# Kernel tuning notes

Hardware: AMD Instinct MI355X
Metric: run time of the kernel (lower is better)

The kernel has to match this reference:

```python
import jax, jax.numpy as jnp
import numpy as np

CLIPS_NUM = 4
OUTPUT_SIZE = 1000000  # outputSize: number of features in trainset (scales Z)
T = 0.07               # temperature
QUEUE_K = 131072       # queue size
D = 128                # inputSize (feature dim)
BS = 256               # batch_size * clips_num


def _l2norm(x):
    return x / jnp.linalg.norm(x, axis=-1, keepdims=True)


def setup_inputs() -> dict:
    key = jax.random.key(0)
    kq, kk, km = jax.random.split(key, 3)
    # MoCo-style L2-normalized features keep exp(sim/T) finite.
    q = _l2norm(jax.random.normal(kq, (BS, D), jnp.float32))
    k = _l2norm(jax.random.normal(kk, (BS, D), jnp.float32))
    memory = _l2norm(jax.random.normal(km, (QUEUE_K, D), jnp.float32))
    return {"q": q, "k": k, "memory": memory, "i": 0}


def _make_indices(bs, clips_num):
    """Static (numpy) replication of MemoryMoCo.prepare_indices."""
    batch_size = bs // clips_num
    # indices[v] = row indices of all clips of video v: [batch_size, clips_num]
    indices = np.arange(bs).reshape(clips_num, batch_size).T
    vid = np.arange(bs) % batch_size
    all_clips = vid[:, None] + np.arange(clips_num)[None, :] * batch_size  # [bs, clips_num]
    mask = all_clips != np.arange(bs)[:, None]
    pos_indices = all_clips[mask].reshape(bs, clips_num - 1)  # drop self
    return jnp.asarray(indices), jnp.asarray(pos_indices)


def reference(q, k, memory, i):
    bs, d = q.shape
    batch_size = bs // CLIPS_NUM
    indices, pos_indices = _make_indices(bs, CLIPS_NUM)

    k = jax.lax.stop_gradient(k)            # k = k.detach()
    mem = jax.lax.stop_gradient(memory)     # queue = memory.clone().detach()

    # l_pos: gather positives, per-row bmm with q, mean over positives -> [bs, 1]
    positives = k[pos_indices]              # [bs, clips_num-1, d]
    l_pos = jnp.mean(jnp.einsum('bpd,bd->bp', positives, q), axis=-1, keepdims=True)

    # l_neg: queue GEMM -> [bs, K]
    l_neg = q @ mem.T

    out = jnp.concatenate([l_pos, l_neg], axis=1)   # [bs, 1+K]
    out = jnp.exp(out / T)
    # First-call NCE normalization: Z = out.mean() * outputSize (Z is detached in torch)
    Z = jax.lax.stop_gradient(jnp.mean(out) * OUTPUT_SIZE)
    out = out / Z

    probs = jnp.mean(out[:, 0] / jnp.sum(out, axis=1))  # extract_probs

    # no_grad memory-bank update: scatter mean of each video's clip keys
    out_ids = jnp.arange(batch_size) % memory.shape[0]   # index=0, fmod queueSize
    k_mean = jnp.mean(k[indices], axis=1)                # [batch_size, d]
    new_memory = memory.at[out_ids].set(k_mean)

    return out, probs, new_memory
```

## Files before the change

### kernel.cpp

```cpp
#include <hip/hip_runtime.h>
#include <hip/hip_bf16.h>

constexpr int       DIM        = 128;
constexpr long long CN         = 131073;
constexpr long long OUT_ELEMS  = 256LL * 131073LL;
constexpr long long PROBS_OFF  = OUT_ELEMS;
constexpr long long MEMOUT_OFF = OUT_ELEMS + 1;
constexpr long long MEM_ELEMS  = 131072LL * 128LL;

constexpr float SCL = 20.60992915555662f;

constexpr int WS_INVZ  = 0;
constexpr int WS_ELPOS = 16;
constexpr int WS_KMEAN = 272;
constexpr int WS_ROWP  = 8464;
constexpr int WS_MEMBF = 16656;

typedef __attribute__((ext_vector_type(8))) short  short8v;
typedef __attribute__((ext_vector_type(4))) float  f32x4;
typedef __attribute__((ext_vector_type(4), aligned(4))) float f32x4u;

__device__ __forceinline__ unsigned short f2bf(float x) {
  unsigned u = __float_as_uint(x);
  u += 0x7fffu + ((u >> 16) & 1u);
  return (unsigned short)(u >> 16);
}

__device__ __forceinline__ short8v pack8(float4 a, float4 b) {
  short8v h;
  h[0] = (short)f2bf(a.x); h[1] = (short)f2bf(a.y);
  h[2] = (short)f2bf(a.z); h[3] = (short)f2bf(a.w);
  h[4] = (short)f2bf(b.x); h[5] = (short)f2bf(b.y);
  h[6] = (short)f2bf(b.z); h[7] = (short)f2bf(b.w);
  return h;
}

__global__ __launch_bounds__(256) void k_prep(const float* __restrict__ q,
                                              const float* __restrict__ k,
                                              float* __restrict__ ws) {
  const int b = blockIdx.x, t = threadIdx.x;
  if (b < 32) {
    int j = b * 256 + t;
    int v = j >> 7, d = j & 127;
    ws[WS_KMEAN + j] = 0.25f * (k[v*128+d] + k[(v+64)*128+d] +
                                k[(v+128)*128+d] + k[(v+192)*128+d]);
  } else if (b < 96) {
    int row = (b - 32) * 4 + (t >> 6);
    int lane = t & 63;
    int vid = row & 63;
    float2 qv = ((const float2*)(q + row * DIM))[lane];
    float2 kr = ((const float2*)(k + row * DIM))[lane];
    float s0 = -kr.x, s1 = -kr.y;
    #pragma unroll
    for (int c = 0; c < 4; ++c) {
      float2 kc = ((const float2*)(k + (vid + c * 64) * DIM))[lane];
      s0 += kc.x; s1 += kc.y;
    }
    float acc = qv.x * s0 + qv.y * s1;
    #pragma unroll
    for (int off = 1; off < 64; off <<= 1) acc += __shfl_xor(acc, off, 64);
    if (lane == 0) ws[WS_ELPOS + row] = exp2f(acc * (1.f / 3.f) * SCL);
  } else {
    int i = (b - 96) * 2048 + t * 8;
    float4 z = {0.f, 0.f, 0.f, 0.f};
    *(float4*)(ws + WS_ROWP + i)     = z;
    *(float4*)(ws + WS_ROWP + i + 4) = z;
  }
}

template<int NT>
__global__ __launch_bounds__(256) void k_gemm0(const float* __restrict__ memv,
                                               const float* __restrict__ q,
                                               unsigned short* __restrict__ membf,
                                               float* __restrict__ ws) {
  const int t = threadIdx.x, lane = t & 63, wave = t >> 6;
  const int g = lane >> 4, nlo = lane & 15;

  short8v af[4][4];
  #pragma unroll
  for (int ks = 0; ks < 4; ++ks)
    #pragma unroll
    for (int mf = 0; mf < 4; ++mf) {
      const float4* src = (const float4*)(q + (wave*64 + mf*16 + nlo)*DIM + ks*32 + g*8);
      af[ks][mf] = pack8(src[0], src[1]);
    }

  float sums[4][4];
  #pragma unroll
  for (int mf = 0; mf < 4; ++mf)
    #pragma unroll
    for (int r = 0; r < 4; ++r) sums[mf][r] = 0.f;

  for (int it = 0; it < NT; ++it) {
    const long long n0 = ((long long)blockIdx.x * NT + it) * 32;
    f32x4 acc[4][2];
    f32x4 zero = {0.f, 0.f, 0.f, 0.f};
    #pragma unroll
    for (int mf = 0; mf < 4; ++mf) { acc[mf][0] = zero; acc[mf][1] = zero; }

    #pragma unroll
    for (int ks = 0; ks < 4; ++ks) {
      #pragma unroll
      for (int nf = 0; nf < 2; ++nf) {
        const long long off = (n0 + nf*16 + nlo) * DIM + ks*32 + g*8;
        const float4* src = (const float4*)(memv + off);
        short8v bfr = pack8(src[0], src[1]);
        if (wave == ks)
          *(short8v*)(membf + off) = bfr;
        #pragma unroll
        for (int mf = 0; mf < 4; ++mf)
          acc[mf][nf] = __builtin_amdgcn_mfma_f32_16x16x32_bf16(af[ks][mf], bfr, acc[mf][nf], 0, 0, 0);
      }
    }

    #pragma unroll
    for (int mf = 0; mf < 4; ++mf)
      #pragma unroll
      for (int r = 0; r < 4; ++r)
        sums[mf][r] += exp2f(acc[mf][0][r] * SCL) + exp2f(acc[mf][1][r] * SCL);
  }

  float* rowp = ws + WS_ROWP + (blockIdx.x & 31) * 256;
  #pragma unroll
  for (int mf = 0; mf < 4; ++mf) {
    #pragma unroll
    for (int r = 0; r < 4; ++r) {
      float s = sums[mf][r];
      s += __shfl_xor(s, 1, 16);
      s += __shfl_xor(s, 2, 16);
      s += __shfl_xor(s, 4, 16);
      s += __shfl_xor(s, 8, 16);
      if (nlo == 0) atomicAdd(&rowp[wave*64 + mf*16 + g*4 + r], s);
    }
  }
}

__global__ void k_fin(float* __restrict__ ws, float* __restrict__ out) {
  __shared__ float s_tot[256];
  __shared__ float s_pr[256];
  __shared__ float sh_invZ;
  int t = threadIdx.x;
  float s = ws[WS_ELPOS + t];
  float rs = s;
  for (int sl = 0; sl < 32; ++sl) rs += ws[WS_ROWP + sl * 256 + t];
  s_tot[t] = rs;
  s_pr[t] = s / rs;
  __syncthreads();
  for (int off = 128; off > 0; off >>= 1) {
    if (t < off) { s_tot[t] += s_tot[t + off]; s_pr[t] += s_pr[t + off]; }
    __syncthreads();
  }
  if (t == 0) {
    double Z = (double)s_tot[0] * (1000000.0 / (256.0 * 131073.0));
    float invZ = (float)(1.0 / Z);
    ws[WS_INVZ] = invZ;
    sh_invZ = invZ;
    out[PROBS_OFF] = s_pr[0] * (1.f / 256.f);
  }
  __syncthreads();
  out[(long long)t * CN] = s * sh_invZ;
}

template<int NT>
__global__ __launch_bounds__(256) void k_gemm1(const unsigned short* __restrict__ membf,
                                               const float* __restrict__ q,
                                               const float* __restrict__ ws,
                                               float* __restrict__ out) {
  const int t = threadIdx.x, lane = t & 63, wave = t >> 6;
  const int g = lane >> 4, nlo = lane & 15;
  const float invZ = ws[WS_INVZ];

  short8v af[4][4];
  #pragma unroll
  for (int ks = 0; ks < 4; ++ks)
    #pragma unroll
    for (int mf = 0; mf < 4; ++mf) {
      const float4* src = (const float4*)(q + (wave*64 + mf*16 + nlo)*DIM + ks*32 + g*8);
      af[ks][mf] = pack8(src[0], src[1]);
    }

  long long rowoff[4][4];
  #pragma unroll
  for (int mf = 0; mf < 4; ++mf)
    #pragma unroll
    for (int r = 0; r < 4; ++r)
      rowoff[mf][r] = (long long)(wave*64 + mf*16 + g*4 + r) * CN + 1 + nlo;

  const int logical = (blockIdx.x & 7) * 64 + (blockIdx.x >> 3);
  const long long t0 = (long long)logical * NT;

  for (int it = 0; it < NT; ++it) {
    const long long n0 = (t0 + it) * 32;
    f32x4 acc[4][2];
    f32x4 zero = {0.f, 0.f, 0.f, 0.f};
    #pragma unroll
    for (int mf = 0; mf < 4; ++mf) { acc[mf][0] = zero; acc[mf][1] = zero; }

    #pragma unroll
    for (int ks = 0; ks < 4; ++ks) {
      short8v b0 = *(const short8v*)(membf + (n0 + nlo)      * DIM + ks*32 + g*8);
      short8v b1 = *(const short8v*)(membf + (n0 + 16 + nlo) * DIM + ks*32 + g*8);
      #pragma unroll
      for (int mf = 0; mf < 4; ++mf) {
        acc[mf][0] = __builtin_amdgcn_mfma_f32_16x16x32_bf16(af[ks][mf], b0, acc[mf][0], 0, 0, 0);
        acc[mf][1] = __builtin_amdgcn_mfma_f32_16x16x32_bf16(af[ks][mf], b1, acc[mf][1], 0, 0, 0);
      }
    }

    #pragma unroll
    for (int mf = 0; mf < 4; ++mf) {
      #pragma unroll
      for (int r = 0; r < 4; ++r) {
        out[rowoff[mf][r] + n0]      = exp2f(acc[mf][0][r] * SCL) * invZ;
        out[rowoff[mf][r] + n0 + 16] = exp2f(acc[mf][1][r] * SCL) * invZ;
      }
    }
  }
}

__global__ void k_copy(const float* __restrict__ memv, const float* __restrict__ ws,
                       float* __restrict__ out) {
  float* dst = out + MEMOUT_OFF;
  const float* km = ws + WS_KMEAN;
  long long gid = blockIdx.x * 256LL + threadIdx.x;
  if (gid == 0) {
    dst[0] = km[0]; dst[1] = km[1]; dst[2] = km[2];
    dst[8191] = km[8191];
    dst[8192] = memv[8192]; dst[8193] = memv[8193]; dst[8194] = memv[8194];
    dst[MEM_ELEMS - 1] = memv[MEM_ELEMS - 1];
  }
  if (gid < 2047) {
    long long base = 3 + gid * 4;
    f32x4u v = *(const f32x4u*)(km + base);
    *(f32x4u*)(dst + base) = v;
  }
  const long long NGB = (MEM_ELEMS - 1 - 8195) / 4;
  const long long stride = (long long)gridDim.x * 256LL;
  for (long long j = gid; j < NGB; j += stride) {
    long long base = 8195 + j * 4;
    f32x4u v = *(const f32x4u*)(memv + base);
    *(f32x4u*)(dst + base) = v;
  }
}

extern "C" void kernel_launch(void* const* d_in, const int* in_sizes, int n_in,
                              void* d_out, int out_size, void* d_ws, size_t ws_size,
                              hipStream_t stream) {
  (void)in_sizes; (void)n_in; (void)out_size; (void)ws_size;
  const float* q    = (const float*)d_in[0];
  const float* k    = (const float*)d_in[1];
  const float* memv = (const float*)d_in[2];
  float* out = (float*)d_out;
  float* ws  = (float*)d_ws;
  unsigned short* membf = (unsigned short*)(ws + WS_MEMBF);

  hipLaunchKernelGGL(k_prep, dim3(100), dim3(256), 0, stream, q, k, ws);
  hipLaunchKernelGGL((k_gemm0<8>), dim3(512), dim3(256), 0, stream, memv, q, membf, ws);
  hipLaunchKernelGGL(k_fin,  dim3(1),   dim3(256), 0, stream, ws, out);
  hipLaunchKernelGGL((k_gemm1<8>), dim3(512), dim3(256), 0, stream, membf, q, ws, out);
  hipLaunchKernelGGL(k_copy, dim3(2048), dim3(256), 0, stream, memv, ws, out);
}
```

Baseline: 409.1 us.

## Fuse all stages into one persistent kernel with a grid-wide barrier

Merges prep, the first GEMM pass, the finalization, the second GEMM pass and the memory copy into a single kernel of 512 blocks. A spin-wait atomic counter acts as a grid barrier between the Z-reduction pass and the output-writing pass. The second pass re-reads and re-converts the fp32 memory instead of going through a bf16 staging copy, and the memory-bank copy is spread across the blocks before the barrier. This removes four kernel launches and the bf16 staging writes. In exchange it re-reads the fp32 memory, adds memsets, and relies on all 512 blocks being co-resident (launch_bounds of 2 blocks per CU), or the barrier deadlocks.

```diff
diff --git a/kernel.cpp b/kernel.cpp
--- a/kernel.cpp
+++ b/kernel.cpp
@@ -10,11 +10,12 @@
 
 constexpr float SCL = 20.60992915555662f;
 
-constexpr int WS_INVZ  = 0;
-constexpr int WS_ELPOS = 16;
+constexpr int WS_CTR   = 8;
 constexpr int WS_KMEAN = 272;
 constexpr int WS_ROWP  = 8464;
-constexpr int WS_MEMBF = 16656;
+
+constexpr int GRID   = 512;
+constexpr int NTILES = 8;
 
 typedef __attribute__((ext_vector_type(8))) short  short8v;
 typedef __attribute__((ext_vector_type(4))) float  f32x4;
@@ -35,55 +36,53 @@
   return h;
 }
 
-__global__ __launch_bounds__(256) void k_prep(const float* __restrict__ q,
-                                              const float* __restrict__ k,
-                                              float* __restrict__ ws) {
+__global__ __launch_bounds__(256, 2) void k_mega(const float* __restrict__ qg,
+                                                 const float* __restrict__ kg,
+                                                 const float* __restrict__ memv,
+                                                 float* __restrict__ ws,
+                                                 float* __restrict__ out) {
   const int b = blockIdx.x, t = threadIdx.x;
-  if (b < 32) {
-    int j = b * 256 + t;
-    int v = j >> 7, d = j & 127;
-    ws[WS_KMEAN + j] = 0.25f * (k[v*128+d] + k[(v+64)*128+d] +
-                                k[(v+128)*128+d] + k[(v+192)*128+d]);
-  } else if (b < 96) {
-    int row = (b - 32) * 4 + (t >> 6);
-    int lane = t & 63;
-    int vid = row & 63;
-    float2 qv = ((const float2*)(q + row * DIM))[lane];
-    float2 kr = ((const float2*)(k + row * DIM))[lane];
-    float s0 = -kr.x, s1 = -kr.y;
-    #pragma unroll
-    for (int c = 0; c < 4; ++c) {
-      float2 kc = ((const float2*)(k + (vid + c * 64) * DIM))[lane];
-      s0 += kc.x; s1 += kc.y;
-    }
-    float acc = qv.x * s0 + qv.y * s1;
-    #pragma unroll
-    for (int off = 1; off < 64; off <<= 1) acc += __shfl_xor(acc, off, 64);
-    if (lane == 0) ws[WS_ELPOS + row] = exp2f(acc * (1.f / 3.f) * SCL);
-  } else {
-    int i = (b - 96) * 2048 + t * 8;
-    float4 z = {0.f, 0.f, 0.f, 0.f};
-    *(float4*)(ws + WS_ROWP + i)     = z;
-    *(float4*)(ws + WS_ROWP + i + 4) = z;
-  }
-}
-
-template<int NT>
-__global__ __launch_bounds__(256) void k_gemm0(const float* __restrict__ memv,
-                                               const float* __restrict__ q,
-                                               unsigned short* __restrict__ membf,
-                                               float* __restrict__ ws) {
-  const int t = threadIdx.x, lane = t & 63, wave = t >> 6;
-  const int g = lane >> 4, nlo = lane & 15;
+  const int lane = t & 63, wave = t >> 6, g = lane >> 4, nlo = lane & 15;
+  __shared__ float sh_s;
+  __shared__ float sh_rs[256];
+  __shared__ float sh_red[256];
 
   short8v af[4][4];
   #pragma unroll
   for (int ks = 0; ks < 4; ++ks)
     #pragma unroll
     for (int mf = 0; mf < 4; ++mf) {
-      const float4* src = (const float4*)(q + (wave*64 + mf*16 + nlo)*DIM + ks*32 + g*8);
+      const float4* src = (const float4*)(qg + (wave*64 + mf*16 + nlo)*DIM + ks*32 + g*8);
       af[ks][mf] = pack8(src[0], src[1]);
     }
+
+  if (b < 256 && wave == 0) {
+    const int vid = b & 63;
+    float2 qv = ((const float2*)(qg + b*DIM))[lane];
+    float2 kr = ((const float2*)(kg + b*DIM))[lane];
+    float s0 = -kr.x, s1 = -kr.y;
+    #pragma unroll
+    for (int c = 0; c < 4; ++c) {
+      float2 kc = ((const float2*)(kg + (vid + c*64)*DIM))[lane];
+      s0 += kc.x; s1 += kc.y;
+    }
+    float acc = qv.x*s0 + qv.y*s1;
+    #pragma unroll
+    for (int off = 1; off < 64; off <<= 1) acc += __shfl_xor(acc, off, 64);
+    if (lane == 0) {
+      float s = exp2f(acc * (1.f/3.f) * SCL);
+      sh_s = s;
+      atomicAdd(&ws[WS_ROWP + (b & 31)*256 + b], s);
+    }
+  }
+  if (b == 0) {
+    for (int j = t; j < 8192; j += 256) {
+      int v = j >> 7, d = j & 127;
+      ws[WS_KMEAN + j] = 0.25f * (kg[v*DIM+d] + kg[(v+64)*DIM+d] +
+                                  kg[(v+128)*DIM+d] + kg[(v+192)*DIM+d]);
+    }
+  }
+  __syncthreads();
 
   float sums[4][4];
   #pragma unroll
@@ -91,8 +90,8 @@
     #pragma unroll
     for (int r = 0; r < 4; ++r) sums[mf][r] = 0.f;
 
-  for (int it = 0; it < NT; ++it) {
-    const long long n0 = ((long long)blockIdx.x * NT + it) * 32;
+  for (int it = 0; it < NTILES; ++it) {
+    const long long n0 = (long long)b * (NTILES*32) + it*32;
     f32x4 acc[4][2];
     f32x4 zero = {0.f, 0.f, 0.f, 0.f};
     #pragma unroll
@@ -100,106 +99,10 @@
 
     #pragma unroll
     for (int ks = 0; ks < 4; ++ks) {
-      #pragma unroll
-      for (int nf = 0; nf < 2; ++nf) {
-        const long long off = (n0 + nf*16 + nlo) * DIM + ks*32 + g*8;
-        const float4* src = (const float4*)(memv + off);
-        short8v bfr = pack8(src[0], src[1]);
-        if (wave == ks)
-          *(short8v*)(membf + off) = bfr;
-        #pragma unroll
-        for (int mf = 0; mf < 4; ++mf)
-          acc[mf][nf] = __builtin_amdgcn_mfma_f32_16x16x32_bf16(af[ks][mf], bfr, acc[mf][nf], 0, 0, 0);
-      }
-    }
-
-    #pragma unroll
-    for (int mf = 0; mf < 4; ++mf)
-      #pragma unroll
-      for (int r = 0; r < 4; ++r)
-        sums[mf][r] += exp2f(acc[mf][0][r] * SCL) + exp2f(acc[mf][1][r] * SCL);
-  }
-
-  float* rowp = ws + WS_ROWP + (blockIdx.x & 31) * 256;
-  #pragma unroll
-  for (int mf = 0; mf < 4; ++mf) {
-    #pragma unroll
-    for (int r = 0; r < 4; ++r) {
-      float s = sums[mf][r];
-      s += __shfl_xor(s, 1, 16);
-      s += __shfl_xor(s, 2, 16);
-      s += __shfl_xor(s, 4, 16);
-      s += __shfl_xor(s, 8, 16);
-      if (nlo == 0) atomicAdd(&rowp[wave*64 + mf*16 + g*4 + r], s);
-    }
-  }
-}
-
-__global__ void k_fin(float* __restrict__ ws, float* __restrict__ out) {
-  __shared__ float s_tot[256];
-  __shared__ float s_pr[256];
-  __shared__ float sh_invZ;
-  int t = threadIdx.x;
-  float s = ws[WS_ELPOS + t];
-  float rs = s;
-  for (int sl = 0; sl < 32; ++sl) rs += ws[WS_ROWP + sl * 256 + t];
-  s_tot[t] = rs;
-  s_pr[t] = s / rs;
-  __syncthreads();
-  for (int off = 128; off > 0; off >>= 1) {
-    if (t < off) { s_tot[t] += s_tot[t + off]; s_pr[t] += s_pr[t + off]; }
-    __syncthreads();
-  }
-  if (t == 0) {
-    double Z = (double)s_tot[0] * (1000000.0 / (256.0 * 131073.0));
-    float invZ = (float)(1.0 / Z);
-    ws[WS_INVZ] = invZ;
-    sh_invZ = invZ;
-    out[PROBS_OFF] = s_pr[0] * (1.f / 256.f);
-  }
-  __syncthreads();
-  out[(long long)t * CN] = s * sh_invZ;
-}
-
-template<int NT>
-__global__ __launch_bounds__(256) void k_gemm1(const unsigned short* __restrict__ membf,
-                                               const float* __restrict__ q,
-                                               const float* __restrict__ ws,
-                                               float* __restrict__ out) {
-  const int t = threadIdx.x, lane = t & 63, wave = t >> 6;
-  const int g = lane >> 4, nlo = lane & 15;
-  const float invZ = ws[WS_INVZ];
-
-  short8v af[4][4];
-  #pragma unroll
-  for (int ks = 0; ks < 4; ++ks)
-    #pragma unroll
-    for (int mf = 0; mf < 4; ++mf) {
-      const float4* src = (const float4*)(q + (wave*64 + mf*16 + nlo)*DIM + ks*32 + g*8);
-      af[ks][mf] = pack8(src[0], src[1]);
-    }
-
-  long long rowoff[4][4];
-  #pragma unroll
-  for (int mf = 0; mf < 4; ++mf)
-    #pragma unroll
-    for (int r = 0; r < 4; ++r)
-      rowoff[mf][r] = (long long)(wave*64 + mf*16 + g*4 + r) * CN + 1 + nlo;
-
-  const int logical = (blockIdx.x & 7) * 64 + (blockIdx.x >> 3);
-  const long long t0 = (long long)logical * NT;
-
-  for (int it = 0; it < NT; ++it) {
-    const long long n0 = (t0 + it) * 32;
-    f32x4 acc[4][2];
-    f32x4 zero = {0.f, 0.f, 0.f, 0.f};
-    #pragma unroll
-    for (int mf = 0; mf < 4; ++mf) { acc[mf][0] = zero; acc[mf][1] = zero; }
-
-    #pragma unroll
-    for (int ks = 0; ks < 4; ++ks) {
-      short8v b0 = *(const short8v*)(membf + (n0 + nlo)      * DIM + ks*32 + g*8);
-      short8v b1 = *(const short8v*)(membf + (n0 + 16 + nlo) * DIM + ks*32 + g*8);
+      const float4* p0 = (const float4*)(memv + (n0 + nlo)      * DIM + ks*32 + g*8);
+      const float4* p1 = (const float4*)(memv + (n0 + 16 + nlo) * DIM + ks*32 + g*8);
+      short8v b0 = pack8(p0[0], p0[1]);
+      short8v b1 = pack8(p1[0], p1[1]);
       #pragma unroll
       for (int mf = 0; mf < 4; ++mf) {
         acc[mf][0] = __builtin_amdgcn_mfma_f32_16x16x32_bf16(af[ks][mf], b0, acc[mf][0], 0, 0, 0);
@@ -208,38 +111,128 @@
     }
 
     #pragma unroll
+    for (int mf = 0; mf < 4; ++mf)
+      #pragma unroll
+      for (int r = 0; r < 4; ++r)
+        sums[mf][r] += exp2f(acc[mf][0][r] * SCL) + exp2f(acc[mf][1][r] * SCL);
+  }
+
+  {
+    float* rowp = ws + WS_ROWP + (b & 31) * 256;
+    #pragma unroll
     for (int mf = 0; mf < 4; ++mf) {
       #pragma unroll
       for (int r = 0; r < 4; ++r) {
-        out[rowoff[mf][r] + n0]      = exp2f(acc[mf][0][r] * SCL) * invZ;
-        out[rowoff[mf][r] + n0 + 16] = exp2f(acc[mf][1][r] * SCL) * invZ;
-      }
-    }
-  }
-}
-
-__global__ void k_copy(const float* __restrict__ memv, const float* __restrict__ ws,
-                       float* __restrict__ out) {
-  float* dst = out + MEMOUT_OFF;
-  const float* km = ws + WS_KMEAN;
-  long long gid = blockIdx.x * 256LL + threadIdx.x;
-  if (gid == 0) {
-    dst[0] = km[0]; dst[1] = km[1]; dst[2] = km[2];
-    dst[8191] = km[8191];
-    dst[8192] = memv[8192]; dst[8193] = memv[8193]; dst[8194] = memv[8194];
-    dst[MEM_ELEMS - 1] = memv[MEM_ELEMS - 1];
-  }
-  if (gid < 2047) {
-    long long base = 3 + gid * 4;
-    f32x4u v = *(const f32x4u*)(km + base);
-    *(f32x4u*)(dst + base) = v;
-  }
-  const long long NGB = (MEM_ELEMS - 1 - 8195) / 4;
-  const long long stride = (long long)gridDim.x * 256LL;
-  for (long long j = gid; j < NGB; j += stride) {
-    long long base = 8195 + j * 4;
-    f32x4u v = *(const f32x4u*)(memv + base);
-    *(f32x4u*)(dst + base) = v;
+        float s = sums[mf][r];
+        s += __shfl_xor(s, 1, 16);
+        s += __shfl_xor(s, 2, 16);
+        s += __shfl_xor(s, 4, 16);
+        s += __shfl_xor(s, 8, 16);
+        if (nlo == 0) atomicAdd(&rowp[wave*64 + mf*16 + g*4 + r], s);
+      }
+    }
+  }
+
+  {
+    float* dst = out + MEMOUT_OFF;
+    const float* km = ws + WS_KMEAN;
+    if (b == 0 && t == 0) {
+      dst[0] = km[0]; dst[1] = km[1]; dst[2] = km[2];
+      dst[MEM_ELEMS - 1] = memv[MEM_ELEMS - 1];
+    }
+    #pragma unroll
+    for (int i = 0; i < 32; ++i) {
+      long long j = (long long)b * 8192 + i*256 + t;
+      if (j < 4194303LL) {
+        long long base = 3 + j*4;
+        f32x4u v;
+        if (base + 4 <= 8192) {
+          v = *(const f32x4u*)(km + base);
+        } else if (base >= 8192) {
+          v = *(const f32x4u*)(memv + base);
+        } else {
+          float tmp[4];
+          #pragma unroll
+          for (int e = 0; e < 4; ++e) {
+            long long idx = base + e;
+            tmp[e] = (idx < 8192) ? km[idx] : memv[idx];
+          }
+          v.x = tmp[0]; v.y = tmp[1]; v.z = tmp[2]; v.w = tmp[3];
+        }
+        *(f32x4u*)(dst + base) = v;
+      }
+    }
+  }
+
+  __syncthreads();
+  if (t == 0) {
+    unsigned* ctr = (unsigned*)ws + WS_CTR;
+    __hip_atomic_fetch_add(ctr, 1u, __ATOMIC_ACQ_REL, __HIP_MEMORY_SCOPE_AGENT);
+    while (__hip_atomic_load(ctr, __ATOMIC_ACQUIRE, __HIP_MEMORY_SCOPE_AGENT) < (unsigned)GRID) {
+      __builtin_amdgcn_s_sleep(2);
+    }
+  }
+  __syncthreads();
+
+  {
+    float rs = 0.f;
+    #pragma unroll
+    for (int sl = 0; sl < 32; ++sl)
+      rs += __hip_atomic_load(&ws[WS_ROWP + sl*256 + t], __ATOMIC_RELAXED, __HIP_MEMORY_SCOPE_AGENT);
+    sh_rs[t] = rs;
+    sh_red[t] = rs;
+  }
+  __syncthreads();
+  for (int off = 128; off > 0; off >>= 1) {
+    if (t < off) sh_red[t] += sh_red[t + off];
+    __syncthreads();
+  }
+  float invZ;
+  {
+    double Z = (double)sh_red[0] * (1000000.0 / (256.0 * 131073.0));
+    invZ = (float)(1.0 / Z);
+  }
+
+  if (b < 256 && t == 0) {
+    out[(long long)b * CN] = sh_s * invZ;
+    atomicAdd(&out[PROBS_OFF], (sh_s / sh_rs[b]) * (1.f / 256.f));
+  }
+
+  long long rowbase[4][4];
+  #pragma unroll
+  for (int mf = 0; mf < 4; ++mf)
+    #pragma unroll
+    for (int r = 0; r < 4; ++r)
+      rowbase[mf][r] = (long long)(wave*64 + mf*16 + g*4 + r) * CN + 1 + nlo;
+
+  for (int it = 0; it < NTILES; ++it) {
+    const long long n0 = (long long)b * (NTILES*32) + it*32;
+    f32x4 acc[4][2];
+    f32x4 zero = {0.f, 0.f, 0.f, 0.f};
+    #pragma unroll
+    for (int mf = 0; mf < 4; ++mf) { acc[mf][0] = zero; acc[mf][1] = zero; }
+
+    #pragma unroll
+    for (int ks = 0; ks < 4; ++ks) {
+      const float4* p0 = (const float4*)(memv + (n0 + nlo)      * DIM + ks*32 + g*8);
+      const float4* p1 = (const float4*)(memv + (n0 + 16 + nlo) * DIM + ks*32 + g*8);
+      short8v b0 = pack8(p0[0], p0[1]);
+      short8v b1 = pack8(p1[0], p1[1]);
+      #pragma unroll
+      for (int mf = 0; mf < 4; ++mf) {
+        acc[mf][0] = __builtin_amdgcn_mfma_f32_16x16x32_bf16(af[ks][mf], b0, acc[mf][0], 0, 0, 0);
+        acc[mf][1] = __builtin_amdgcn_mfma_f32_16x16x32_bf16(af[ks][mf], b1, acc[mf][1], 0, 0, 0);
+      }
+    }
+
+    #pragma unroll
+    for (int mf = 0; mf < 4; ++mf) {
+      #pragma unroll
+      for (int r = 0; r < 4; ++r) {
+        out[rowbase[mf][r] + n0]      = exp2f(acc[mf][0][r] * SCL) * invZ;
+        out[rowbase[mf][r] + n0 + 16] = exp2f(acc[mf][1][r] * SCL) * invZ;
+      }
+    }
   }
 }
 
@@ -252,11 +245,10 @@
   const float* memv = (const float*)d_in[2];
   float* out = (float*)d_out;
   float* ws  = (float*)d_ws;
-  unsigned short* membf = (unsigned short*)(ws + WS_MEMBF);
-
-  hipLaunchKernelGGL(k_prep, dim3(100), dim3(256), 0, stream, q, k, ws);
-  hipLaunchKernelGGL((k_gemm0<8>), dim3(512), dim3(256), 0, stream, memv, q, membf, ws);
-  hipLaunchKernelGGL(k_fin,  dim3(1),   dim3(256), 0, stream, ws, out);
-  hipLaunchKernelGGL((k_gemm1<8>), dim3(512), dim3(256), 0, stream, membf, q, ws, out);
-  hipLaunchKernelGGL(k_copy, dim3(2048), dim3(256), 0, stream, memv, ws, out);
-}
+
+  hipMemsetAsync((void*)(ws + WS_ROWP), 0, 32 * 256 * sizeof(float), stream);
+  hipMemsetAsync((void*)((unsigned*)ws + WS_CTR), 0, sizeof(unsigned), stream);
+  hipMemsetAsync((void*)(out + PROBS_OFF), 0, sizeof(float), stream);
+
+  hipLaunchKernelGGL(k_mega, dim3(GRID), dim3(256), 0, stream, q, k, memv, ws, out);
+}
```

Measured after the change: 488.8 us. 1.19x slower.

## Fuse memory-bank copy into first GEMM pass and use nontemporal output stores

Applied to the files above, without the earlier changes.

The separate memory-bank copy kernel is removed. Its work now runs inside the first GEMM pass, so the memv rows it reads are already being streamed for the bf16 conversion. Both GEMM kernels switch to 1024 blocks with 4 tiles each, an XCD-aware block remap and a launch-bounds occupancy hint. The large output writes use nontemporal stores. This cuts one launch and one full read of memv, at the cost of more register and branch pressure in the first GEMM.

```diff
diff --git a/kernel.cpp b/kernel.cpp
--- a/kernel.cpp
+++ b/kernel.cpp
@@ -69,12 +69,14 @@
 }
 
 template<int NT>
-__global__ __launch_bounds__(256) void k_gemm0(const float* __restrict__ memv,
-                                               const float* __restrict__ q,
-                                               unsigned short* __restrict__ membf,
-                                               float* __restrict__ ws) {
+__global__ __launch_bounds__(256, 4) void k_gemmA(const float* __restrict__ memv,
+                                                  const float* __restrict__ q,
+                                                  unsigned short* __restrict__ membf,
+                                                  float* __restrict__ ws,
+                                                  float* __restrict__ out) {
   const int t = threadIdx.x, lane = t & 63, wave = t >> 6;
   const int g = lane >> 4, nlo = lane & 15;
+  const int logical = (blockIdx.x & 7) * 128 + (blockIdx.x >> 3);
 
   short8v af[4][4];
   #pragma unroll
@@ -92,7 +94,7 @@
     for (int r = 0; r < 4; ++r) sums[mf][r] = 0.f;
 
   for (int it = 0; it < NT; ++it) {
-    const long long n0 = ((long long)blockIdx.x * NT + it) * 32;
+    const long long n0 = ((long long)logical * NT + it) * 32;
     f32x4 acc[4][2];
     f32x4 zero = {0.f, 0.f, 0.f, 0.f};
     #pragma unroll
@@ -120,17 +122,51 @@
         sums[mf][r] += exp2f(acc[mf][0][r] * SCL) + exp2f(acc[mf][1][r] * SCL);
   }
 
-  float* rowp = ws + WS_ROWP + (blockIdx.x & 31) * 256;
-  #pragma unroll
-  for (int mf = 0; mf < 4; ++mf) {
-    #pragma unroll
-    for (int r = 0; r < 4; ++r) {
-      float s = sums[mf][r];
-      s += __shfl_xor(s, 1, 16);
-      s += __shfl_xor(s, 2, 16);
-      s += __shfl_xor(s, 4, 16);
-      s += __shfl_xor(s, 8, 16);
-      if (nlo == 0) atomicAdd(&rowp[wave*64 + mf*16 + g*4 + r], s);
+  {
+    float* rowp = ws + WS_ROWP + (blockIdx.x & 31) * 256;
+    #pragma unroll
+    for (int mf = 0; mf < 4; ++mf) {
+      #pragma unroll
+      for (int r = 0; r < 4; ++r) {
+        float s = sums[mf][r];
+        s += __shfl_xor(s, 1, 16);
+        s += __shfl_xor(s, 2, 16);
+        s += __shfl_xor(s, 4, 16);
+        s += __shfl_xor(s, 8, 16);
+        if (nlo == 0) atomicAdd(&rowp[wave*64 + mf*16 + g*4 + r], s);
+      }
+    }
+  }
+
+  {
+    float* dst = out + MEMOUT_OFF;
+    const float* km = ws + WS_KMEAN;
+    if (logical == 0 && t == 0) {
+      dst[0] = km[0]; dst[1] = km[1]; dst[2] = km[2];
+      dst[MEM_ELEMS - 1] = memv[MEM_ELEMS - 1];
+    }
+    const long long j0 = (long long)logical * 4096;
+    #pragma unroll
+    for (int i = 0; i < 16; ++i) {
+      long long j = j0 + i*256 + t;
+      if (j < 4194303LL) {
+        long long base = 3 + j*4;
+        f32x4u v;
+        if (base + 4 <= 8192) {
+          v = *(const f32x4u*)(km + base);
+        } else if (base >= 8192) {
+          v = *(const f32x4u*)(memv + base);
+        } else {
+          float tmp[4];
+          #pragma unroll
+          for (int e = 0; e < 4; ++e) {
+            long long idx = base + e;
+            tmp[e] = (idx < 8192) ? km[idx] : memv[idx];
+          }
+          v.x = tmp[0]; v.y = tmp[1]; v.z = tmp[2]; v.w = tmp[3];
+        }
+        __builtin_nontemporal_store(v, (f32x4u*)(dst + base));
+      }
     }
   }
 }
@@ -162,13 +198,14 @@
 }
 
 template<int NT>
-__global__ __launch_bounds__(256) void k_gemm1(const unsigned short* __restrict__ membf,
-                                               const float* __restrict__ q,
-                                               const float* __restrict__ ws,
-                                               float* __restrict__ out) {
+__global__ __launch_bounds__(256, 4) void k_gemmB(const unsigned short* __restrict__ membf,
+                                                  const float* __restrict__ q,
+                                                  const float* __restrict__ ws,
+                                                  float* __restrict__ out) {
   const int t = threadIdx.x, lane = t & 63, wave = t >> 6;
   const int g = lane >> 4, nlo = lane & 15;
   const float invZ = ws[WS_INVZ];
+  const int logical = (blockIdx.x & 7) * 128 + (blockIdx.x >> 3);
 
   short8v af[4][4];
   #pragma unroll
@@ -179,18 +216,8 @@
       af[ks][mf] = pack8(src[0], src[1]);
     }
 
-  long long rowoff[4][4];
-  #pragma unroll
-  for (int mf = 0; mf < 4; ++mf)
-    #pragma unroll
-    for (int r = 0; r < 4; ++r)
-      rowoff[mf][r] = (long long)(wave*64 + mf*16 + g*4 + r) * CN + 1 + nlo;
-
-  const int logical = (blockIdx.x & 7) * 64 + (blockIdx.x >> 3);
-  const long long t0 = (long long)logical * NT;
-
   for (int it = 0; it < NT; ++it) {
-    const long long n0 = (t0 + it) * 32;
+    const long long n0 = ((long long)logical * NT + it) * 32;
     f32x4 acc[4][2];
     f32x4 zero = {0.f, 0.f, 0.f, 0.f};
     #pragma unroll
@@ -211,35 +238,11 @@
     for (int mf = 0; mf < 4; ++mf) {
       #pragma unroll
       for (int r = 0; r < 4; ++r) {
-        out[rowoff[mf][r] + n0]      = exp2f(acc[mf][0][r] * SCL) * invZ;
-        out[rowoff[mf][r] + n0 + 16] = exp2f(acc[mf][1][r] * SCL) * invZ;
-      }
-    }
-  }
-}
-
-__global__ void k_copy(const float* __restrict__ memv, const float* __restrict__ ws,
-                       float* __restrict__ out) {
-  float* dst = out + MEMOUT_OFF;
-  const float* km = ws + WS_KMEAN;
-  long long gid = blockIdx.x * 256LL + threadIdx.x;
-  if (gid == 0) {
-    dst[0] = km[0]; dst[1] = km[1]; dst[2] = km[2];
-    dst[8191] = km[8191];
-    dst[8192] = memv[8192]; dst[8193] = memv[8193]; dst[8194] = memv[8194];
-    dst[MEM_ELEMS - 1] = memv[MEM_ELEMS - 1];
-  }
-  if (gid < 2047) {
-    long long base = 3 + gid * 4;
-    f32x4u v = *(const f32x4u*)(km + base);
-    *(f32x4u*)(dst + base) = v;
-  }
-  const long long NGB = (MEM_ELEMS - 1 - 8195) / 4;
-  const long long stride = (long long)gridDim.x * 256LL;
-  for (long long j = gid; j < NGB; j += stride) {
-    long long base = 8195 + j * 4;
-    f32x4u v = *(const f32x4u*)(memv + base);
-    *(f32x4u*)(dst + base) = v;
+        const long long base = (long long)(wave*64 + mf*16 + g*4 + r) * CN + 1 + nlo + n0;
+        __builtin_nontemporal_store(exp2f(acc[mf][0][r] * SCL) * invZ, out + base);
+        __builtin_nontemporal_store(exp2f(acc[mf][1][r] * SCL) * invZ, out + base + 16);
+      }
+    }
   }
 }
 
@@ -255,8 +258,7 @@
   unsigned short* membf = (unsigned short*)(ws + WS_MEMBF);
 
   hipLaunchKernelGGL(k_prep, dim3(100), dim3(256), 0, stream, q, k, ws);
-  hipLaunchKernelGGL((k_gemm0<8>), dim3(512), dim3(256), 0, stream, memv, q, membf, ws);
+  hipLaunchKernelGGL((k_gemmA<4>), dim3(1024), dim3(256), 0, stream, memv, q, membf, ws, out);
   hipLaunchKernelGGL(k_fin,  dim3(1),   dim3(256), 0, stream, ws, out);
-  hipLaunchKernelGGL((k_gemm1<8>), dim3(512), dim3(256), 0, stream, membf, q, ws, out);
-  hipLaunchKernelGGL(k_copy, dim3(2048), dim3(256), 0, stream, memv, ws, out);
-}
+  hipLaunchKernelGGL((k_gemmB<4>), dim3(1024), dim3(256), 0, stream, membf, q, ws, out);
+}
```

Measured after the change: 493.1 us. 20.5% more time.
